# Optimization experiments

Measured on AMD Instinct MI355X. Metric: run time of the kernel, lower is better.

## Reference

```python
import jax, jax.numpy as jnp
import numpy as np

MARGIN = 0.5

def setup_inputs() -> dict:
    key = jax.random.key(0)
    k1, k2, k3, k4 = jax.random.split(key, 4)
    B, C, T, K = 16, 512, 2048, 4096
    student_out = jax.random.normal(k1, (B, C, T), dtype=jnp.float32)
    teacher_out = jax.random.normal(k2, (B, C, T), dtype=jnp.float32)
    codebook = jax.random.normal(k3, (K, C), dtype=jnp.float32)
    teacher_codes = jax.random.randint(k4, (B, T), 0, K, dtype=jnp.int64)
    return {"student_out": student_out, "teacher_out": teacher_out,
            "codebook": codebook, "teacher_codes": teacher_codes}

def _hard_negatives(student_out, codebook, teacher_codes):
    B, C, T = student_out.shape
    z = jnp.transpose(student_out, (0, 2, 1)).reshape(-1, C)  # (B*T, C)
    # squared Euclidean via expansion; sqrt-free suffices for argmin but keep faithful masking
    sq = (jnp.sum(z * z, axis=1, keepdims=True)
          + jnp.sum(codebook * codebook, axis=1)[None, :]
          - 2.0 * z @ codebook.T)                              # (B*T, K)
    dists = jnp.sqrt(jnp.maximum(sq, 0.0))
    tflat = teacher_codes.reshape(-1)
    rows = jnp.arange(tflat.shape[0])
    dists = dists.at[rows, tflat].set(jnp.inf)                 # mask correct code
    hard_idx = jnp.argmin(dists, axis=1)                       # (B*T,)
    return codebook[hard_idx].reshape(B, T, C)

def reference(student_out, teacher_out, codebook, teacher_codes):
    B, C, T = student_out.shape
    negative = _hard_negatives(student_out, codebook, teacher_codes)  # (B, T, C)
    anchor = jnp.transpose(teacher_out, (0, 2, 1))   # (B, T, C)
    positive = jnp.transpose(student_out, (0, 2, 1)) # (B, T, C)
    d_pos = jnp.linalg.norm(anchor - positive, axis=-1)  # (B, T)
    d_neg = jnp.linalg.norm(anchor - negative, axis=-1)  # (B, T)
    losses = jax.nn.relu(d_pos - d_neg + MARGIN)
    loss = losses.mean()
    d_pos_mean = d_pos.mean()
    d_neg_mean = d_neg.mean()
    margin_satisfied = (d_neg > d_pos + MARGIN).astype(jnp.float32).mean()
    return (loss, d_pos_mean, d_neg_mean, margin_satisfied)
```

## Files before the change

### kernel.cpp

```cpp
#include <hip/hip_runtime.h>
#include <math.h>

#define B_ 16
#define C_ 512
#define T_ 2048
#define K_ 4096
#define M_ (B_*T_)
#define MARGIN_ 0.5f

typedef float f32x4 __attribute__((ext_vector_type(4)));
typedef long  longx2 __attribute__((ext_vector_type(2)));

static __device__ __forceinline__ unsigned int umin_(unsigned int a, unsigned int b) {
    return a < b ? a : b;
}
static __device__ __forceinline__ unsigned int umax_(unsigned int a, unsigned int b) {
    return a > b ? a : b;
}
static __device__ __forceinline__ void gload_lds16(const void* g, void* l) {
    __builtin_amdgcn_global_load_lds(
        (const __attribute__((address_space(1))) unsigned int*)g,
        (__attribute__((address_space(3))) unsigned int*)l,
        16, 0, 0);
}

static __device__ __forceinline__ unsigned char f32_to_e4m3(float x) {
    unsigned int u = __float_as_uint(x);
    unsigned int sgn = (u >> 24) & 0x80u;
    unsigned int ax = u & 0x7FFFFFFFu;
    if (ax >= 0x43E00000u) return (unsigned char)(sgn | 0x7Eu);
    if (ax < 0x3C800000u) {
        int q = (int)rintf(__uint_as_float(ax) * 512.0f);
        if (q >= 8) return (unsigned char)(sgn | 0x08u);
        return (unsigned char)(sgn | (unsigned)q);
    }
    unsigned int b = ax + 0x7FFFFu + ((ax >> 20) & 1u);
    unsigned int e = b >> 23;
    unsigned int m = (b >> 20) & 7u;
    int e4 = (int)e - 127 + 7;
    if (e4 >= 16) return (unsigned char)(sgn | 0x7Eu);
    return (unsigned char)(sgn | ((unsigned)e4 << 3) | m);
}

static __device__ __forceinline__ int ileave8(int pi) {
    return ((pi & 3) * 2 + (pi >> 2)) * 8;
}

__global__ __launch_bounds__(256) void packA_kernel(
    const float* __restrict__ student, unsigned char* __restrict__ Apack)
{
    __shared__ float ts[64][65];
    const int tid = threadIdx.x;
    const int t0 = blockIdx.x * 64;
    const int c0 = blockIdx.y * 64;
    const int b  = blockIdx.z;

#pragma unroll
    for (int r = 0; r < 4; ++r) {
        int f  = tid + r * 256;
        int i  = f >> 4;
        int j4 = (f & 15) << 2;
        float4 v = *reinterpret_cast<const float4*>(
            student + ((size_t)(b * C_ + c0 + i)) * T_ + (t0 + j4));
        *reinterpret_cast<float4*>(&ts[i][j4]) = v;
    }
    __syncthreads();

#pragma unroll
    for (int r = 0; r < 2; ++r) {
        int f  = tid + r * 256;
        int j  = f >> 3;
        int pi = f & 7;
        unsigned long long w = 0ull;
#pragma unroll
        for (int u = 0; u < 8; ++u) {
            unsigned long long byte8 = (unsigned long long)f32_to_e4m3(ts[pi * 8 + u][j]);
            w |= byte8 << (8 * u);
        }
        *reinterpret_cast<unsigned long long*>(
            Apack + (size_t)(b * T_ + t0 + j) * 512 + c0 + ileave8(pi)) = w;
    }
}

__global__ __launch_bounds__(256) void packB_norm_kernel(
    const float* __restrict__ cb, unsigned char* __restrict__ Bpack,
    float* __restrict__ cbnb256)
{
    int code = blockIdx.x * 4 + (threadIdx.x >> 6);
    int lane = threadIdx.x & 63;
    const float* row = cb + (size_t)code * C_;
    unsigned char* orow = Bpack + (size_t)code * 512;

    int c = lane * 8;
    float4 v0 = *reinterpret_cast<const float4*>(row + c);
    float4 v1 = *reinterpret_cast<const float4*>(row + c + 4);
    float s = v0.x*v0.x + v0.y*v0.y + v0.z*v0.z + v0.w*v0.w
            + v1.x*v1.x + v1.y*v1.y + v1.z*v1.z + v1.w*v1.w;
    unsigned long long w =
          (unsigned long long)f32_to_e4m3(v0.x)
        | ((unsigned long long)f32_to_e4m3(v0.y) << 8)
        | ((unsigned long long)f32_to_e4m3(v0.z) << 16)
        | ((unsigned long long)f32_to_e4m3(v0.w) << 24)
        | ((unsigned long long)f32_to_e4m3(v1.x) << 32)
        | ((unsigned long long)f32_to_e4m3(v1.y) << 40)
        | ((unsigned long long)f32_to_e4m3(v1.z) << 48)
        | ((unsigned long long)f32_to_e4m3(v1.w) << 56);
    *reinterpret_cast<unsigned long long*>(
        orow + (lane >> 3) * 64 + ileave8(lane & 7)) = w;

#pragma unroll
    for (int off = 32; off; off >>= 1) s += __shfl_down(s, off);
    if (lane == 0) cbnb256[code] = (s + 1024.0f) * 256.0f;
}

__global__ __launch_bounds__(256, 2) void screen_kernel(
    const unsigned char* __restrict__ Apack,
    const unsigned char* __restrict__ Bpack,
    const float* __restrict__ cbnb256,
    uint2* __restrict__ out2)
{
    __shared__ __align__(16) unsigned char lds_tiles[4 * 2 * 128 * 64];
    __shared__ float cbnb_lds[1024];

    const int tid = threadIdx.x;
    const int l   = tid & 63;
    const int wv  = tid >> 6;
    const int wm  = wv >> 1, wn = wv & 1;
    const int lr  = l & 15;
    const int lk  = l >> 4;

    const int bid = blockIdx.x;
    const int wg  = (bid & 7) * 128 + (bid >> 3);
    const int q   = wg & 3;
    const int m0  = (wg >> 2) * 128;

    {
        float4 v = reinterpret_cast<const float4*>(cbnb256 + q * 1024)[tid];
        reinterpret_cast<float4*>(cbnb_lds)[tid] = v;
    }

    unsigned int u1[16], u2v[16];
#pragma unroll
    for (int e = 0; e < 16; ++e) { u1[e] = 0xFFFFFFFFu; u2v[e] = 0xFFFFFFFFu; }

    f32x4 acc[4][4];
#pragma unroll
    for (int i = 0; i < 4; ++i)
#pragma unroll
        for (int j = 0; j < 4; ++j) acc[i][j] = (f32x4)0.f;

    const int lane_goff = (l >> 2) * 512 + (((l & 3) ^ ((l >> 3) & 3)) * 16);
    const int r0 = wv * 32, r1 = wv * 32 + 16;

    const char* pA0 = (const char*)Apack + (size_t)m0 * 512 + lane_goff + (size_t)r0 * 512;
    const char* pA1 = (const char*)Apack + (size_t)m0 * 512 + lane_goff + (size_t)r1 * 512;
    const char* pB0 = (const char*)Bpack + (size_t)q * 524288 + lane_goff + (size_t)r0 * 512;
    const char* pB1 = (const char*)Bpack + (size_t)q * 524288 + lane_goff + (size_t)r1 * 512;

    auto stage_ptr = [&](unsigned bufbase) {
        unsigned char* Ad = &lds_tiles[bufbase];
        unsigned char* Bd = &lds_tiles[bufbase + 8192];
        gload_lds16(pA0, Ad + r0 * 64);
        gload_lds16(pA1, Ad + r1 * 64);
        gload_lds16(pB0, Bd + r0 * 64);
        gload_lds16(pB1, Bd + r1 * 64);
    };
    auto advance = [&](int s_next) {
        bool wrap = (s_next & 7) == 0;
        int dA = wrap ? -448 : 64;
        int dB = wrap ? 65088 : 64;
        pA0 += dA; pA1 += dA; pB0 += dB; pB1 += dB;
    };

    const int slotoff = (lk ^ ((lr >> 1) & 3)) * 16;

    auto compute_step = [&](unsigned bufbase) {
        longx2 a[4], bb[4];
#pragma unroll
        for (int i = 0; i < 4; ++i) {
            int ar = wm * 64 + i * 16 + lr;
            a[i]  = *reinterpret_cast<const longx2*>(
                        &lds_tiles[bufbase + ar * 64 + slotoff]);
            int br = wn * 64 + i * 16 + lr;
            bb[i] = *reinterpret_cast<const longx2*>(
                        &lds_tiles[bufbase + 8192 + br * 64 + slotoff]);
        }
#pragma unroll
        for (int i = 0; i < 4; ++i)
#pragma unroll
            for (int j = 0; j < 4; ++j) {
                acc[i][j] = __builtin_amdgcn_mfma_f32_16x16x32_fp8_fp8(
                    a[i][0], bb[j][0], acc[i][j], 0, 0, 0);
                acc[i][j] = __builtin_amdgcn_mfma_f32_16x16x32_fp8_fp8(
                    a[i][1], bb[j][1], acc[i][j], 0, 0, 0);
            }
    };

    auto fold = [&](int ct) {
        unsigned int kk4[4];
        float cnb[4];
#pragma unroll
        for (int j = 0; j < 4; ++j) {
            int kl = ct * 128 + wn * 64 + j * 16 + lr;
            kk4[j] = (unsigned int)(q * 1024 + kl);
            cnb[j] = cbnb_lds[kl];
        }
#pragma unroll
        for (int i = 0; i < 4; ++i)
#pragma unroll
            for (int r = 0; r < 4; ++r) {
                int e = i * 4 + r;
                unsigned int p[4];
#pragma unroll
                for (int j = 0; j < 4; ++j) {
                    float s = fmaf(-512.f, acc[i][j][r], cnb[j]);
                    s = fmaxf(s, 0.f);
                    p[j] = ((unsigned int)s << 12) | kk4[j];
                }
                unsigned int mn0 = umin_(p[0], p[1]), mx0 = umax_(p[0], p[1]);
                unsigned int mn1 = umin_(p[2], p[3]), mx1 = umax_(p[2], p[3]);
                unsigned int t0 = umax_(u1[e], mn0);
                u1[e]  = umin_(u1[e], mn0);
                u2v[e] = umin_(umin_(t0, u2v[e]), mx0);
                unsigned int t1 = umax_(u1[e], mn1);
                u1[e]  = umin_(u1[e], mn1);
                u2v[e] = umin_(umin_(t1, u2v[e]), mx1);
            }
#pragma unroll
        for (int i = 0; i < 4; ++i)
#pragma unroll
            for (int j = 0; j < 4; ++j) acc[i][j] = (f32x4)0.f;
    };

    stage_ptr(0u);        advance(1);
    stage_ptr(16384u);    advance(2);

    for (int w = 0; w < 32; ++w) {
        asm volatile("s_waitcnt vmcnt(0)" ::: "memory");
        __builtin_amdgcn_s_barrier();

        if (w < 31) {
            int s2 = 2 * w + 2;
            stage_ptr((unsigned)((s2 & 3) * 16384));       advance(s2 + 1);
            stage_ptr((unsigned)(((s2 + 1) & 3) * 16384)); advance(s2 + 2);
        }

        compute_step((unsigned)(((2 * w) & 3) * 16384));
        compute_step((unsigned)(((2 * w + 1) & 3) * 16384));
        if ((w & 3) == 3) fold(w >> 2);
    }

#pragma unroll
    for (int e = 0; e < 16; ++e) {
        unsigned int a1 = u1[e], a2 = u2v[e];
#pragma unroll
        for (int off = 1; off < 16; off <<= 1) {
            unsigned int b1 = (unsigned int)__shfl_xor((int)a1, off);
            unsigned int b2 = (unsigned int)__shfl_xor((int)a2, off);
            unsigned int m1 = umin_(a1, b1);
            a2 = umin_(umax_(a1, b1), umin_(a2, b2));
            a1 = m1;
        }
        u1[e] = a1; u2v[e] = a2;
    }

    if (lr == 0) {
        int cand = q * 2 + wn;
#pragma unroll
        for (int i = 0; i < 4; ++i)
#pragma unroll
            for (int r = 0; r < 4; ++r) {
                int m = m0 + wm * 64 + i * 16 + lk * 4 + r;
                out2[(size_t)cand * M_ + m] = make_uint2(u1[i * 4 + r], u2v[i * 4 + r]);
            }
    }
}

__global__ __launch_bounds__(256) void loss_kernel(
    const float* __restrict__ student, const float* __restrict__ teacher,
    const float* __restrict__ cb, const uint2* __restrict__ out2,
    const int* __restrict__ codes, float* __restrict__ partials)
{
    __shared__ float sh[4][64][5];

    const int l  = threadIdx.x & 63;
    const int qw = threadIdx.x >> 6;
    const int m  = blockIdx.x * 64 + l;
    const int b  = m / T_;
    const int t  = m % T_;

    uint2 g = out2[m];
#pragma unroll
    for (int c = 1; c < 8; ++c) {
        uint2 o = out2[(size_t)c * M_ + m];
        unsigned int m1 = umin_(g.x, o.x);
        g.y = umin_(umax_(g.x, o.x), umin_(g.y, o.y));
        g.x = m1;
    }
    const int k1 = (int)(g.x & 0xFFFu);
    const int k2 = (int)(g.y & 0xFFFu);

    const float* sp = student + (size_t)b * C_ * T_ + t;
    const float* tp = teacher + (size_t)b * C_ * T_ + t;
    const float4* c1p = reinterpret_cast<const float4*>(cb + (size_t)k1 * C_);
    const float4* c2p = reinterpret_cast<const float4*>(cb + (size_t)k2 * C_);

    float dp = 0.f, ds1 = 0.f, ds2 = 0.f, dt1 = 0.f, dt2 = 0.f;
    const int c4beg = qw * 32;
#pragma unroll 4
    for (int c4 = c4beg; c4 < c4beg + 32; ++c4) {
        float4 cv1 = c1p[c4];
        float4 cv2 = c2p[c4];
        float a0 = tp[(size_t)(c4 * 4 + 0) * T_];
        float a1 = tp[(size_t)(c4 * 4 + 1) * T_];
        float a2 = tp[(size_t)(c4 * 4 + 2) * T_];
        float a3 = tp[(size_t)(c4 * 4 + 3) * T_];
        float p0 = sp[(size_t)(c4 * 4 + 0) * T_];
        float p1 = sp[(size_t)(c4 * 4 + 1) * T_];
        float p2 = sp[(size_t)(c4 * 4 + 2) * T_];
        float p3 = sp[(size_t)(c4 * 4 + 3) * T_];
        float e;
        e = a0 - p0;   dp  = fmaf(e, e, dp);
        e = a1 - p1;   dp  = fmaf(e, e, dp);
        e = a2 - p2;   dp  = fmaf(e, e, dp);
        e = a3 - p3;   dp  = fmaf(e, e, dp);
        e = p0 - cv1.x; ds1 = fmaf(e, e, ds1);
        e = p1 - cv1.y; ds1 = fmaf(e, e, ds1);
        e = p2 - cv1.z; ds1 = fmaf(e, e, ds1);
        e = p3 - cv1.w; ds1 = fmaf(e, e, ds1);
        e = p0 - cv2.x; ds2 = fmaf(e, e, ds2);
        e = p1 - cv2.y; ds2 = fmaf(e, e, ds2);
        e = p2 - cv2.z; ds2 = fmaf(e, e, ds2);
        e = p3 - cv2.w; ds2 = fmaf(e, e, ds2);
        e = a0 - cv1.x; dt1 = fmaf(e, e, dt1);
        e = a1 - cv1.y; dt1 = fmaf(e, e, dt1);
        e = a2 - cv1.z; dt1 = fmaf(e, e, dt1);
        e = a3 - cv1.w; dt1 = fmaf(e, e, dt1);
        e = a0 - cv2.x; dt2 = fmaf(e, e, dt2);
        e = a1 - cv2.y; dt2 = fmaf(e, e, dt2);
        e = a2 - cv2.z; dt2 = fmaf(e, e, dt2);
        e = a3 - cv2.w; dt2 = fmaf(e, e, dt2);
    }
    sh[qw][l][0] = dp;
    sh[qw][l][1] = ds1;
    sh[qw][l][2] = ds2;
    sh[qw][l][3] = dt1;
    sh[qw][l][4] = dt2;
    __syncthreads();

    if (qw == 0) {
        float S0 = 0.f, S1 = 0.f, S2 = 0.f, S3 = 0.f, S4 = 0.f;
#pragma unroll
        for (int w = 0; w < 4; ++w) {
            S0 += sh[w][l][0];
            S1 += sh[w][l][1];
            S2 += sh[w][l][2];
            S3 += sh[w][l][3];
            S4 += sh[w][l][4];
        }
        const int tc = codes[m];
        bool v1 = (k1 != tc), v2 = (k2 != tc);
        bool take2;
        if (!v1)      take2 = true;
        else if (!v2) take2 = false;
        else          take2 = (S2 < S1) || (S2 == S1 && k2 < k1);
        float dn = take2 ? S4 : S3;

        float dpos = sqrtf(S0);
        float dneg = sqrtf(dn);
        float loss = fmaxf(dpos - dneg + MARGIN_, 0.f);
        float ind  = (dneg > dpos + MARGIN_) ? 1.f : 0.f;

        float v0 = loss, vv1 = dpos, vv2 = dneg, vv3 = ind;
#pragma unroll
        for (int off = 32; off; off >>= 1) {
            v0  += __shfl_down(v0, off);
            vv1 += __shfl_down(vv1, off);
            vv2 += __shfl_down(vv2, off);
            vv3 += __shfl_down(vv3, off);
        }
        if (l == 0) {
            partials[blockIdx.x * 4 + 0] = v0;
            partials[blockIdx.x * 4 + 1] = vv1;
            partials[blockIdx.x * 4 + 2] = vv2;
            partials[blockIdx.x * 4 + 3] = vv3;
        }
    }
}

__global__ __launch_bounds__(256) void final_kernel(
    const float* __restrict__ partials, float* __restrict__ out)
{
    __shared__ float sh[4][4];
    int tid = threadIdx.x;
    float s0 = partials[tid * 4 + 0] + partials[(tid + 256) * 4 + 0];
    float s1 = partials[tid * 4 + 1] + partials[(tid + 256) * 4 + 1];
    float s2 = partials[tid * 4 + 2] + partials[(tid + 256) * 4 + 2];
    float s3 = partials[tid * 4 + 3] + partials[(tid + 256) * 4 + 3];
#pragma unroll
    for (int off = 32; off; off >>= 1) {
        s0 += __shfl_down(s0, off);
        s1 += __shfl_down(s1, off);
        s2 += __shfl_down(s2, off);
        s3 += __shfl_down(s3, off);
    }
    int w = tid >> 6, lane = tid & 63;
    if (lane == 0) { sh[w][0] = s0; sh[w][1] = s1; sh[w][2] = s2; sh[w][3] = s3; }
    __syncthreads();
    if (tid == 0) {
        const float inv = 1.0f / (float)M_;
        float o0 = 0.f, o1 = 0.f, o2 = 0.f, o3 = 0.f;
#pragma unroll
        for (int ww = 0; ww < 4; ++ww) {
            o0 += sh[ww][0]; o1 += sh[ww][1]; o2 += sh[ww][2]; o3 += sh[ww][3];
        }
        out[0] = o0 * inv;
        out[1] = o1 * inv;
        out[2] = o2 * inv;
        out[3] = o3 * inv;
    }
}

extern "C" void kernel_launch(void* const* d_in, const int* in_sizes, int n_in,
                              void* d_out, int out_size, void* d_ws, size_t ws_size,
                              hipStream_t stream)
{
    (void)in_sizes; (void)n_in; (void)out_size; (void)ws_size;
    const float* student = (const float*)d_in[0];
    const float* teacher = (const float*)d_in[1];
    const float* cb      = (const float*)d_in[2];
    const int*   codes   = (const int*)d_in[3];
    float* out = (float*)d_out;
    char* ws = (char*)d_ws;

    const size_t OFF_APACK = 0;
    const size_t OFF_BPACK = (size_t)M_ * 512;
    const size_t OFF_CBN   = OFF_BPACK + (size_t)K_ * 512;
    const size_t OFF_OUT2  = OFF_CBN + K_ * 4;
    const size_t OFF_PARTS = OFF_OUT2 + (size_t)8 * M_ * 8;

    unsigned char* Apack = (unsigned char*)(ws + OFF_APACK);
    unsigned char* Bpack = (unsigned char*)(ws + OFF_BPACK);
    float* cbnb  = (float*)(ws + OFF_CBN);
    uint2* out2  = (uint2*)(ws + OFF_OUT2);
    float* parts = (float*)(ws + OFF_PARTS);

    packA_kernel<<<dim3(T_ / 64, C_ / 64, B_), 256, 0, stream>>>(student, Apack);
    packB_norm_kernel<<<K_ / 4, 256, 0, stream>>>(cb, Bpack, cbnb);
    screen_kernel<<<1024, 256, 0, stream>>>(Apack, Bpack, cbnb, out2);
    loss_kernel<<<M_ / 64, 256, 0, stream>>>(student, teacher, cb, out2, codes, parts);
    final_kernel<<<1, 256, 0, stream>>>(parts, out);
}
```

Baseline: 169.4 us.

## Use 16x16x128 scaled FP8 MFMA with full B panel in LDS and direct A loads

Replaces the double-buffered 64-byte K-slice pipeline with a loop over code tiles. Each tile loads a full 128x512 FP8 codebook panel into LDS with an XOR swizzle, while A fragments are read directly from global memory into registers. The products now use the gfx950 16x16x128 scaled f8f6f4 MFMA with unit scales instead of pairs of 16x16x32 FP8 MFMAs, and the pack kernels drop the interleaved byte layout. The intent is fewer MFMA issues and fewer barriers per K. The cost is loss of load/compute overlap, because each panel is loaded and synchronised before compute, plus repeated uncached global A reads and a larger LDS footprint that may limit occupancy.

```diff
diff --git a/kernel.cpp b/kernel.cpp
--- a/kernel.cpp
+++ b/kernel.cpp
@@ -8,8 +8,9 @@
 #define M_ (B_*T_)
 #define MARGIN_ 0.5f
 
-typedef float f32x4 __attribute__((ext_vector_type(4)));
-typedef long  longx2 __attribute__((ext_vector_type(2)));
+typedef float f32x4   __attribute__((ext_vector_type(4)));
+typedef int   int32x4v __attribute__((ext_vector_type(4)));
+typedef int   int32x8v __attribute__((ext_vector_type(8)));
 
 static __device__ __forceinline__ unsigned int umin_(unsigned int a, unsigned int b) {
     return a < b ? a : b;
@@ -42,10 +43,6 @@
     return (unsigned char)(sgn | ((unsigned)e4 << 3) | m);
 }
 
-static __device__ __forceinline__ int ileave8(int pi) {
-    return ((pi & 3) * 2 + (pi >> 2)) * 8;
-}
-
 __global__ __launch_bounds__(256) void packA_kernel(
     const float* __restrict__ student, unsigned char* __restrict__ Apack)
 {
@@ -78,7 +75,7 @@
             w |= byte8 << (8 * u);
         }
         *reinterpret_cast<unsigned long long*>(
-            Apack + (size_t)(b * T_ + t0 + j) * 512 + c0 + ileave8(pi)) = w;
+            Apack + (size_t)(b * T_ + t0 + j) * 512 + c0 + pi * 8) = w;
     }
 }
 
@@ -105,8 +102,7 @@
         | ((unsigned long long)f32_to_e4m3(v1.y) << 40)
         | ((unsigned long long)f32_to_e4m3(v1.z) << 48)
         | ((unsigned long long)f32_to_e4m3(v1.w) << 56);
-    *reinterpret_cast<unsigned long long*>(
-        orow + (lane >> 3) * 64 + ileave8(lane & 7)) = w;
+    *reinterpret_cast<unsigned long long*>(orow + c) = w;
 
 #pragma unroll
     for (int off = 32; off; off >>= 1) s += __shfl_down(s, off);
@@ -119,7 +115,7 @@
     const float* __restrict__ cbnb256,
     uint2* __restrict__ out2)
 {
-    __shared__ __align__(16) unsigned char lds_tiles[4 * 2 * 128 * 64];
+    __shared__ __align__(16) unsigned char bpanel[128 * 512];
     __shared__ float cbnb_lds[1024];
 
     const int tid = threadIdx.x;
@@ -149,52 +145,11 @@
 #pragma unroll
         for (int j = 0; j < 4; ++j) acc[i][j] = (f32x4)0.f;
 
-    const int lane_goff = (l >> 2) * 512 + (((l & 3) ^ ((l >> 3) & 3)) * 16);
-    const int r0 = wv * 32, r1 = wv * 32 + 16;
-
-    const char* pA0 = (const char*)Apack + (size_t)m0 * 512 + lane_goff + (size_t)r0 * 512;
-    const char* pA1 = (const char*)Apack + (size_t)m0 * 512 + lane_goff + (size_t)r1 * 512;
-    const char* pB0 = (const char*)Bpack + (size_t)q * 524288 + lane_goff + (size_t)r0 * 512;
-    const char* pB1 = (const char*)Bpack + (size_t)q * 524288 + lane_goff + (size_t)r1 * 512;
-
-    auto stage_ptr = [&](unsigned bufbase) {
-        unsigned char* Ad = &lds_tiles[bufbase];
-        unsigned char* Bd = &lds_tiles[bufbase + 8192];
-        gload_lds16(pA0, Ad + r0 * 64);
-        gload_lds16(pA1, Ad + r1 * 64);
-        gload_lds16(pB0, Bd + r0 * 64);
-        gload_lds16(pB1, Bd + r1 * 64);
-    };
-    auto advance = [&](int s_next) {
-        bool wrap = (s_next & 7) == 0;
-        int dA = wrap ? -448 : 64;
-        int dB = wrap ? 65088 : 64;
-        pA0 += dA; pA1 += dA; pB0 += dB; pB1 += dB;
-    };
-
-    const int slotoff = (lk ^ ((lr >> 1) & 3)) * 16;
-
-    auto compute_step = [&](unsigned bufbase) {
-        longx2 a[4], bb[4];
-#pragma unroll
-        for (int i = 0; i < 4; ++i) {
-            int ar = wm * 64 + i * 16 + lr;
-            a[i]  = *reinterpret_cast<const longx2*>(
-                        &lds_tiles[bufbase + ar * 64 + slotoff]);
-            int br = wn * 64 + i * 16 + lr;
-            bb[i] = *reinterpret_cast<const longx2*>(
-                        &lds_tiles[bufbase + 8192 + br * 64 + slotoff]);
-        }
-#pragma unroll
-        for (int i = 0; i < 4; ++i)
-#pragma unroll
-            for (int j = 0; j < 4; ++j) {
-                acc[i][j] = __builtin_amdgcn_mfma_f32_16x16x32_fp8_fp8(
-                    a[i][0], bb[j][0], acc[i][j], 0, 0, 0);
-                acc[i][j] = __builtin_amdgcn_mfma_f32_16x16x32_fp8_fp8(
-                    a[i][1], bb[j][1], acc[i][j], 0, 0, 0);
-            }
-    };
+    const unsigned char* pA = Apack + (size_t)(m0 + wm * 64 + lr) * 512 + lk * 32;
+
+    const int h  = l >> 5;
+    const int s5 = l & 31;
+    const unsigned char* Bq = Bpack + (size_t)q * 524288;
 
     auto fold = [&](int ct) {
         unsigned int kk4[4];
@@ -232,22 +187,44 @@
             for (int j = 0; j < 4; ++j) acc[i][j] = (f32x4)0.f;
     };
 
-    stage_ptr(0u);        advance(1);
-    stage_ptr(16384u);    advance(2);
-
-    for (int w = 0; w < 32; ++w) {
-        asm volatile("s_waitcnt vmcnt(0)" ::: "memory");
-        __builtin_amdgcn_s_barrier();
-
-        if (w < 31) {
-            int s2 = 2 * w + 2;
-            stage_ptr((unsigned)((s2 & 3) * 16384));       advance(s2 + 1);
-            stage_ptr((unsigned)(((s2 + 1) & 3) * 16384)); advance(s2 + 2);
-        }
-
-        compute_step((unsigned)(((2 * w) & 3) * 16384));
-        compute_step((unsigned)(((2 * w + 1) & 3) * 16384));
-        if ((w & 3) == 3) fold(w >> 2);
+    for (int ct = 0; ct < 8; ++ct) {
+        __syncthreads();
+        const unsigned char* Bct = Bq + (size_t)ct * 65536;
+#pragma unroll
+        for (int r2 = 0; r2 < 16; ++r2) {
+            int Rbase = wv * 32 + r2 * 2;
+            int row   = Rbase + h;
+            int goff  = (s5 ^ (row & 7)) * 16;
+            gload_lds16(Bct + (size_t)row * 512 + goff, &bpanel[Rbase * 512]);
+        }
+        __syncthreads();
+
+#pragma unroll
+        for (int seg = 0; seg < 4; ++seg) {
+            int32x8v a[4], bb[4];
+#pragma unroll
+            for (int i = 0; i < 4; ++i)
+                a[i] = *reinterpret_cast<const int32x8v*>(
+                    pA + (size_t)i * 8192 + seg * 128);
+#pragma unroll
+            for (int j = 0; j < 4; ++j) {
+                int br  = wn * 64 + j * 16 + lr;
+                int key = br & 7;
+                int g0  = seg * 8 + ((2 * lk) ^ key);
+                int g1  = seg * 8 + ((2 * lk + 1) ^ key);
+                const unsigned char* bp = &bpanel[br * 512];
+                int32x4v blo = *reinterpret_cast<const int32x4v*>(bp + g0 * 16);
+                int32x4v bhi = *reinterpret_cast<const int32x4v*>(bp + g1 * 16);
+                bb[j] = __builtin_shufflevector(blo, bhi, 0, 1, 2, 3, 4, 5, 6, 7);
+            }
+#pragma unroll
+            for (int i = 0; i < 4; ++i)
+#pragma unroll
+                for (int j = 0; j < 4; ++j)
+                    acc[i][j] = __builtin_amdgcn_mfma_scale_f32_16x16x128_f8f6f4(
+                        a[i], bb[j], acc[i][j], 0, 0, 0, 127, 0, 127);
+        }
+        fold(ct);
     }
 
 #pragma unroll
```

After: 184.4 us. +8.8%, slower.
